# Performance work log

Measured on AMD Instinct MI355X. Metric: run time of the kernel, lower is better.

Reference implementation:

```python
import jax, jax.numpy as jnp
import numpy as np

L = 16384      # sequence length
D_IN = 512     # d_input
D_H = 1024     # d_hidden
D_OUT = 512    # d_output
R_MIN = 0.0
R_MAX = 0.99
MAX_PHASE = np.pi


def setup_inputs() -> dict:
    key = jax.random.key(0)
    k_nu, k_th, k_x, k_bre, k_bim, k_cre, k_cim, k_d = jax.random.split(key, 8)
    # nu_init with parametrization='exp'
    u_nu = jax.random.uniform(k_nu, (D_H,), dtype=jnp.float32)
    nu = jnp.sqrt(u_nu * (R_MAX ** 2 - R_MIN ** 2) + R_MIN ** 2)
    u_theta = jax.random.uniform(k_th, (D_H,), dtype=jnp.float32, minval=-MAX_PHASE, maxval=MAX_PHASE)
    theta = jnp.mod(u_theta, 2 * jnp.pi)
    lamb = jnp.stack([jnp.log(-jnp.log(nu)), jnp.log(theta)], axis=0)  # [2, D_H]
    # gamma_init with parametrization='exp': nu = exp(-exp(lamb[0]))
    nu_eff = jnp.exp(-jnp.exp(lamb[0]))
    gamma = jnp.log(jnp.sqrt(1.0 - jnp.abs(nu_eff) ** 2))  # [D_H]
    # matrix_init: normal / sqrt(shape[0])
    B_re = jax.random.normal(k_bre, (D_H, D_IN), dtype=jnp.float32) / jnp.sqrt(D_H)
    B_im = jax.random.normal(k_bim, (D_H, D_IN), dtype=jnp.float32) / jnp.sqrt(D_H)
    C_re = jax.random.normal(k_cre, (D_OUT, D_H), dtype=jnp.float32) / jnp.sqrt(D_OUT)
    C_im = jax.random.normal(k_cim, (D_OUT, D_H), dtype=jnp.float32) / jnp.sqrt(D_OUT)
    D = jax.random.normal(k_d, (D_OUT, D_IN), dtype=jnp.float32) / jnp.sqrt(D_OUT)
    inputs = jax.random.normal(k_x, (L, D_IN), dtype=jnp.float32)
    return {"inputs": inputs, "lamb": lamb, "gamma": gamma,
            "B_re": B_re, "B_im": B_im, "C_re": C_re, "C_im": C_im, "D": D}


def _binary_operator_diag(q_i, q_j):
    A_i, b_i = q_i
    A_j, b_j = q_j
    return (A_j * A_i, A_j * b_i + b_j)


def reference(inputs, lamb, gamma, B_re, B_im, C_re, C_im, D):
    # parametrization='exp': lambda = exp(-exp(nu_log) + i*exp(theta_log))
    diag_lambda = jnp.exp(-jnp.exp(lamb[0]) + 1j * jnp.exp(lamb[1]))  # [D_H] complex64
    # which_gamma='learned', exp param: scale rows of B by exp(gamma)
    B_norm = jnp.exp(gamma)[:, None] * (B_re + 1j * B_im)             # [D_H, D_IN]
    # Bu_t = B_norm @ x_t for all t, as one GEMM: [L, D_H] complex
    Bu = inputs.astype(B_norm.dtype) @ B_norm.T
    Lambda_elements = jnp.broadcast_to(diag_lambda[None, :], Bu.shape)
    # diagonal linear recurrence h_t = lambda*h_{t-1} + Bu_t via parallel scan
    _, h = jax.lax.associative_scan(_binary_operator_diag, (Lambda_elements, Bu))
    C = C_re + 1j * C_im
    # y_t = Re[C h_t] + D x_t
    outputs = jnp.real(h @ C.T) + inputs @ D.T  # [L, D_OUT]
    return outputs
```

## Files before the change

kernel.cpp:

```cpp
#include <hip/hip_runtime.h>

__device__ __forceinline__ unsigned short f2b(float f) {
    unsigned int u = __builtin_bit_cast(unsigned int, f);
    unsigned int r = (u + 0x7FFFu + ((u >> 16) & 1u)) >> 16;
    return (unsigned short)r;
}
__device__ __forceinline__ float b2f(unsigned short s) {
    unsigned int u = ((unsigned int)s) << 16;
    return __builtin_bit_cast(float, u);
}

typedef __attribute__((ext_vector_type(8))) short short8;
typedef __attribute__((ext_vector_type(4))) float float4v;

#define GLD16(g, l) __builtin_amdgcn_global_load_lds(                          \
    (const __attribute__((address_space(1))) unsigned int*)(g),                \
    (__attribute__((address_space(3))) unsigned int*)(l), 16, 0, 0)

#define WAIT_VMN(n)  __builtin_amdgcn_s_waitcnt(0x0F70 | (n))
#define SB()         __builtin_amdgcn_sched_barrier(0)
#define BAR()        __builtin_amdgcn_s_barrier()

#define SEQLEN 16384
#define NCHUNK 512
#define TCHUNK 32
#define LDH 2560

__global__ void prep_all(const float* __restrict__ x,
                         const float* __restrict__ B_re, const float* __restrict__ B_im,
                         const float* __restrict__ gamma,
                         const float* __restrict__ C_re, const float* __restrict__ C_im,
                         const float* __restrict__ Dm,
                         unsigned short* __restrict__ Hcat,
                         unsigned short* __restrict__ Bcat,
                         unsigned short* __restrict__ CW,
                         float* __restrict__ Yzero) {
    int b = blockIdx.x;
    if (b < 8192) {
        int id = b * 256 + threadIdx.x;
        int t = id >> 7;
        int k4 = (id & 127) << 2;
        float4 v = *(const float4*)(x + (long)t * 512 + k4);
        ushort4 o;
        o.x = f2b(v.x); o.y = f2b(v.y); o.z = f2b(v.z); o.w = f2b(v.w);
        *(ushort4*)(Hcat + (long)t * LDH + 2048 + k4) = o;
    } else if (b < 9216) {
        int id = (b - 8192) * 256 + threadIdx.x;
        int n = id >> 7;
        int k4 = (id & 127) << 2;
        const float* src = (n < 1024) ? (B_re + (long)n * 512) : (B_im + (long)(n - 1024) * 512);
        float g = expf(gamma[n & 1023]);
        float4 v = *(const float4*)(src + k4);
        ushort4 o;
        o.x = f2b(v.x * g); o.y = f2b(v.y * g); o.z = f2b(v.z * g); o.w = f2b(v.w * g);
        *(ushort4*)(Bcat + (long)n * 512 + k4) = o;
    } else if (b < 10496) {
        int id = (b - 9216) * 256 + threadIdx.x;
        int o = id / 640;
        int j4 = (id - o * 640) << 2;
        float4 v; float sgn = 1.0f;
        if (j4 < 1024) {
            v = *(const float4*)(C_re + (long)o * 1024 + j4);
        } else if (j4 < 2048) {
            v = *(const float4*)(C_im + (long)o * 1024 + (j4 - 1024));
            sgn = -1.0f;
        } else {
            v = *(const float4*)(Dm + (long)o * 512 + (j4 - 2048));
        }
        ushort4 w;
        w.x = f2b(v.x * sgn); w.y = f2b(v.y * sgn); w.z = f2b(v.z * sgn); w.w = f2b(v.w * sgn);
        *(ushort4*)(CW + (long)o * 2560 + j4) = w;
    } else {
        int id = (b - 10496) * 256 + threadIdx.x;
        float4 z = {0.0f, 0.0f, 0.0f, 0.0f};
        *(float4*)(Yzero + (long)id * 4) = z;
    }
}

template <int EPI>
__device__ __forceinline__ void gemm256_body(
        const unsigned short* __restrict__ A, int lda,
        const unsigned short* __restrict__ B, int ldb,
        void* __restrict__ Cout, int ldc,
        int nk, long kbase, long m0, long n0) {
    constexpr int ASH = 16384;
    __shared__ unsigned short sm[2][32768] __attribute__((aligned(16)));

    const int tid  = threadIdx.x;
    const int lane = tid & 63;
    const int wid  = tid >> 6;
    const int wr   = wid >> 2;
    const int wc   = wid & 3;

    const int sr = lane >> 3;
    const int sc = ((lane & 7) ^ sr) << 3;
    const unsigned short* Agl = A + (m0 + sr) * (long)lda + sc + kbase;
    const unsigned short* Bgl = B + (n0 + sr) * (long)ldb + sc + kbase;

    const int fr = lane & 15;
    const int x7 = fr & 7;
    const int k0off = (((lane >> 4)    ) ^ x7) << 3;
    const int k1off = (((lane >> 4) + 4) ^ x7) << 3;

    float4v acc[8][4] = {};
    short8 fa[4][2];
    short8 fb[4][2];

    auto stageB = [&](unsigned short* buf, long kt) {
        unsigned short* ldsB = buf + ASH + wid * 512;
        const unsigned short* gB = Bgl + kt;
#pragma unroll
        for (int i = 0; i < 4; i++)
            GLD16(gB + (long)(8 * (wid + 8 * i)) * ldb, ldsB + i * 4096);
    };
    auto stageA = [&](unsigned short* buf, long kt) {
        unsigned short* ldsA = buf + wid * 512;
        const unsigned short* gA = Agl + kt;
#pragma unroll
        for (int i = 0; i < 4; i++)
            GLD16(gA + (long)(8 * (wid + 8 * i)) * lda, ldsA + i * 4096);
    };
    auto ldA = [&](const unsigned short* buf, int mbase) {
#pragma unroll
        for (int i = 0; i < 4; i++) {
            const unsigned short* p = buf + (wr * 128 + (mbase + i) * 16 + fr) * 64;
            fa[i][0] = *(const short8*)(p + k0off);
            fa[i][1] = *(const short8*)(p + k1off);
        }
    };
    auto ldB = [&](const unsigned short* buf, int nbase) {
#pragma unroll
        for (int j = 0; j < 2; j++) {
            const unsigned short* p = buf + ASH + (wc * 64 + (nbase + j) * 16 + fr) * 64;
            fb[nbase + j][0] = *(const short8*)(p + k0off);
            fb[nbase + j][1] = *(const short8*)(p + k1off);
        }
    };
    auto mfmaQ = [&](int mbase, int nbase) {
        __builtin_amdgcn_s_setprio(1);
#pragma unroll
        for (int i = 0; i < 4; i++)
#pragma unroll
            for (int j = 0; j < 2; j++) {
                acc[mbase + i][nbase + j] = __builtin_amdgcn_mfma_f32_16x16x32_bf16(
                    fa[i][0], fb[nbase + j][0], acc[mbase + i][nbase + j], 0, 0, 0);
                acc[mbase + i][nbase + j] = __builtin_amdgcn_mfma_f32_16x16x32_bf16(
                    fa[i][1], fb[nbase + j][1], acc[mbase + i][nbase + j], 0, 0, 0);
            }
        __builtin_amdgcn_s_setprio(0);
    };

    stageB(sm[0], 0);  stageA(sm[0], 0);
    stageB(sm[1], 64); stageA(sm[1], 64);
    WAIT_VMN(8);
    SB(); BAR(); SB();

    for (int t = 0; t < nk; ++t) {
        unsigned short* cur = sm[t & 1];
        const bool st = (t + 2 < nk);
        const long kt2 = (long)(t + 2) * 64;
        ldA(cur, 0); ldB(cur, 0);
        SB(); BAR(); SB();
        mfmaQ(0, 0);
        SB(); BAR(); SB();
        ldB(cur, 2);
        SB(); BAR(); SB();
        mfmaQ(0, 2);
        SB(); BAR(); SB();
        if (st) stageB(cur, kt2);
        ldA(cur, 4);
        SB(); BAR(); SB();
        mfmaQ(4, 0);
        SB(); BAR(); SB();
        if (st) stageA(cur, kt2);
        SB();
        mfmaQ(4, 2);
        if (st)              WAIT_VMN(8);
        else if (t + 1 < nk) WAIT_VMN(0);
        SB(); BAR(); SB();
    }

    const int er = (lane >> 4) * 4;
    const int ec = lane & 15;
#pragma unroll
    for (int mi = 0; mi < 8; mi++) {
#pragma unroll
        for (int r = 0; r < 4; r++) {
            long grow = m0 + wr * 128 + mi * 16 + er + r;
#pragma unroll
            for (int nj = 0; nj < 4; nj++) {
                long gcol = n0 + wc * 64 + nj * 16 + ec;
                float v = acc[mi][nj][r];
                if (EPI == 0)
                    ((unsigned short*)Cout)[grow * ldc + gcol] = f2b(v);
                else
                    atomicAdd(&((float*)Cout)[grow * ldc + gcol], v);
            }
        }
    }
}

__global__ __launch_bounds__(512, 1)
void gemm_bu(const unsigned short* __restrict__ A, int lda,
             const unsigned short* __restrict__ B, int ldb,
             void* __restrict__ Cout, int ldc) {
    const int bid = blockIdx.x;
    const int l = (bid & 7) * 64 + (bid >> 3);
    const long m0 = (long)(l >> 3) * 256;
    const long n0 = (long)(l & 7) * 256;
    gemm256_body<0>(A, lda, B, ldb, Cout, ldc, 8, 0, m0, n0);
}

__global__ __launch_bounds__(512, 1)
void gemm_y(const unsigned short* __restrict__ A, int lda,
            const unsigned short* __restrict__ B, int ldb,
            void* __restrict__ Cout, int ldc) {
    const int bid = blockIdx.x;
    const int l = (bid & 7) * 32 + (bid >> 3);
    const long kbase = (long)(l & 1) * 1280;
    const long n0 = (long)((l >> 1) & 1) * 256;
    const long m0 = (long)(l >> 2) * 256;
    gemm256_body<1>(A, lda, B, ldb, Cout, ldc, 20, kbase, m0, n0);
}

__global__ void scan_ends(const unsigned short* __restrict__ Hcat,
                          const float* __restrict__ lamb,
                          float* __restrict__ E) {
    const int chunk = blockIdx.x;
    const int ch = threadIdx.x << 2;
    float lre[4], lim[4];
#pragma unroll
    for (int i = 0; i < 4; i++) {
        float nu = expf(-expf(lamb[ch + i]));
        float th = expf(lamb[1024 + ch + i]);
        lre[i] = nu * cosf(th);
        lim[i] = nu * sinf(th);
    }
    float hr[4] = {0, 0, 0, 0}, hi[4] = {0, 0, 0, 0};
    const unsigned short* base = Hcat + (long)chunk * TCHUNK * LDH + ch;
#pragma unroll 4
    for (int t = 0; t < TCHUNK; t++) {
        ushort4 br = *(const ushort4*)(base + (long)t * LDH);
        ushort4 bi = *(const ushort4*)(base + (long)t * LDH + 1024);
        float brf[4] = {b2f(br.x), b2f(br.y), b2f(br.z), b2f(br.w)};
        float bif[4] = {b2f(bi.x), b2f(bi.y), b2f(bi.z), b2f(bi.w)};
#pragma unroll
        for (int i = 0; i < 4; i++) {
            float nr = fmaf(lre[i], hr[i], fmaf(-lim[i], hi[i], brf[i]));
            float ni = fmaf(lre[i], hi[i], fmaf(lim[i], hr[i], bif[i]));
            hr[i] = nr; hi[i] = ni;
        }
    }
    float* Ec = E + (long)chunk * 2048 + ch;
#pragma unroll
    for (int i = 0; i < 4; i++) {
        Ec[i] = hr[i];
        Ec[1024 + i] = hi[i];
    }
}

__global__ void carry(const float* __restrict__ lamb, const float* __restrict__ E,
                      float* __restrict__ Kc) {
    const int lane = threadIdx.x & 63;
    const int ch = blockIdx.x * 4 + (threadIdx.x >> 6);
    double nu = exp(-exp((double)lamb[ch]));
    double th = exp((double)lamb[1024 + ch]);
    double lr = nu * cos(th), li = nu * sin(th);
#pragma unroll
    for (int i = 0; i < 5; i++) {
        double rr = lr * lr - li * li;
        double ii = 2.0 * lr * li;
        lr = rr; li = ii;
    }
    const float tre = (float)lr, tim = (float)li;
    double ar = lr, ai = li;
#pragma unroll
    for (int i = 0; i < 3; i++) {
        double rr = ar * ar - ai * ai;
        double ii = 2.0 * ar * ai;
        ar = rr; ai = ii;
    }
    float Ar = (float)ar, Ai = (float)ai;

    const int c0 = lane * 8;
    float er[8], ei[8];
#pragma unroll
    for (int j = 0; j < 8; j++) {
        er[j] = E[(long)(c0 + j) * 2048 + ch];
        ei[j] = E[(long)(c0 + j) * 2048 + 1024 + ch];
    }
    float hr = 0.0f, hi = 0.0f;
#pragma unroll
    for (int j = 0; j < 8; j++) {
        float nr = fmaf(tre, hr, fmaf(-tim, hi, er[j]));
        float ni = fmaf(tre, hi, fmaf(tim, hr, ei[j]));
        hr = nr; hi = ni;
    }
#pragma unroll
    for (int o = 1; o < 64; o <<= 1) {
        float pr = __shfl_up(hr, o);
        float pi = __shfl_up(hi, o);
        float qr = __shfl_up(Ar, o);
        float qi = __shfl_up(Ai, o);
        if (lane >= o) {
            float nr = fmaf(Ar, pr, fmaf(-Ai, pi, hr));
            float ni = fmaf(Ar, pi, fmaf(Ai, pr, hi));
            hr = nr; hi = ni;
            float nar = Ar * qr - Ai * qi;
            float nai = Ar * qi + Ai * qr;
            Ar = nar; Ai = nai;
        }
    }
    float sr = __shfl_up(hr, 1);
    float si = __shfl_up(hi, 1);
    if (lane == 0) { sr = 0.0f; si = 0.0f; }
#pragma unroll
    for (int j = 0; j < 8; j++) {
        Kc[(long)(c0 + j) * 2048 + ch] = sr;
        Kc[(long)(c0 + j) * 2048 + 1024 + ch] = si;
        float nr = fmaf(tre, sr, fmaf(-tim, si, er[j]));
        float ni = fmaf(tre, si, fmaf(tim, sr, ei[j]));
        sr = nr; si = ni;
    }
}

__global__ void scan_apply(unsigned short* __restrict__ Hcat,
                           const float* __restrict__ lamb,
                           const float* __restrict__ Kc) {
    const int chunk = blockIdx.x;
    const int ch = threadIdx.x << 2;
    float lre[4], lim[4];
#pragma unroll
    for (int i = 0; i < 4; i++) {
        float nu = expf(-expf(lamb[ch + i]));
        float th = expf(lamb[1024 + ch + i]);
        lre[i] = nu * cosf(th);
        lim[i] = nu * sinf(th);
    }
    float hr[4], hi[4];
#pragma unroll
    for (int i = 0; i < 4; i++) {
        hr[i] = Kc[(long)chunk * 2048 + ch + i];
        hi[i] = Kc[(long)chunk * 2048 + 1024 + ch + i];
    }
    unsigned short* base = Hcat + (long)chunk * TCHUNK * LDH + ch;
#pragma unroll 4
    for (int t = 0; t < TCHUNK; t++) {
        ushort4 br = *(const ushort4*)(base + (long)t * LDH);
        ushort4 bi = *(const ushort4*)(base + (long)t * LDH + 1024);
        float brf[4] = {b2f(br.x), b2f(br.y), b2f(br.z), b2f(br.w)};
        float bif[4] = {b2f(bi.x), b2f(bi.y), b2f(bi.z), b2f(bi.w)};
#pragma unroll
        for (int i = 0; i < 4; i++) {
            float nr = fmaf(lre[i], hr[i], fmaf(-lim[i], hi[i], brf[i]));
            float ni = fmaf(lre[i], hi[i], fmaf(lim[i], hr[i], bif[i]));
            hr[i] = nr; hi[i] = ni;
        }
        ushort4 orv, oiv;
        orv.x = f2b(hr[0]); orv.y = f2b(hr[1]); orv.z = f2b(hr[2]); orv.w = f2b(hr[3]);
        oiv.x = f2b(hi[0]); oiv.y = f2b(hi[1]); oiv.z = f2b(hi[2]); oiv.w = f2b(hi[3]);
        *(ushort4*)(base + (long)t * LDH) = orv;
        *(ushort4*)(base + (long)t * LDH + 1024) = oiv;
    }
}

extern "C" void kernel_launch(void* const* d_in, const int* in_sizes, int n_in,
                              void* d_out, int out_size, void* d_ws, size_t ws_size,
                              hipStream_t stream) {
    const float* x     = (const float*)d_in[0];
    const float* lamb  = (const float*)d_in[1];
    const float* gamma = (const float*)d_in[2];
    const float* B_re  = (const float*)d_in[3];
    const float* B_im  = (const float*)d_in[4];
    const float* C_re  = (const float*)d_in[5];
    const float* C_im  = (const float*)d_in[6];
    const float* Dm    = (const float*)d_in[7];

    char* ws = (char*)d_ws;
    unsigned short* Hcat = (unsigned short*)ws;
    float* E  = (float*)(ws + 83886080);
    float* Kc = E + (long)NCHUNK * 2048;
    unsigned short* Bcat = (unsigned short*)((char*)Kc + 4194304);
    unsigned short* CW   = Bcat + (long)2048 * 512;

    prep_all<<<12544, 256, 0, stream>>>(x, B_re, B_im, gamma, C_re, C_im, Dm,
                                        Hcat, Bcat, CW, (float*)d_out);
    gemm_bu<<<512, 512, 0, stream>>>(Hcat + 2048, LDH, Bcat, 512, Hcat, LDH);
    scan_ends<<<NCHUNK, 256, 0, stream>>>(Hcat, lamb, E);
    carry<<<256, 256, 0, stream>>>(lamb, E, Kc);
    scan_apply<<<NCHUNK, 256, 0, stream>>>(Hcat, lamb, Kc);
    gemm_y<<<256, 512, 0, stream>>>(Hcat, LDH, CW, 2560, (float*)d_out, 512);
}
```

Before: 274.8 us.

## Fuse scan kernels with grid barrier and drop split-K atomics in output GEMM

```diff
diff --git a/kernel.cpp b/kernel.cpp
--- a/kernel.cpp
+++ b/kernel.cpp
@@ -34,7 +34,7 @@
                          unsigned short* __restrict__ Hcat,
                          unsigned short* __restrict__ Bcat,
                          unsigned short* __restrict__ CW,
-                         float* __restrict__ Yzero) {
+                         unsigned int* __restrict__ ctr) {
     int b = blockIdx.x;
     if (b < 8192) {
         int id = b * 256 + threadIdx.x;
@@ -71,18 +71,14 @@
         w.x = f2b(v.x * sgn); w.y = f2b(v.y * sgn); w.z = f2b(v.z * sgn); w.w = f2b(v.w * sgn);
         *(ushort4*)(CW + (long)o * 2560 + j4) = w;
     } else {
-        int id = (b - 10496) * 256 + threadIdx.x;
-        float4 z = {0.0f, 0.0f, 0.0f, 0.0f};
-        *(float4*)(Yzero + (long)id * 4) = z;
-    }
-}
-
-template <int EPI>
-__device__ __forceinline__ void gemm256_body(
-        const unsigned short* __restrict__ A, int lda,
-        const unsigned short* __restrict__ B, int ldb,
-        void* __restrict__ Cout, int ldc,
-        int nk, long kbase, long m0, long n0) {
+        if (threadIdx.x < 2) ctr[threadIdx.x] = 0u;
+    }
+}
+
+__global__ __launch_bounds__(512, 1)
+void gemm_bu(const unsigned short* __restrict__ A, int lda,
+             const unsigned short* __restrict__ B, int ldb,
+             unsigned short* __restrict__ Cout, int ldc) {
     constexpr int ASH = 16384;
     __shared__ unsigned short sm[2][32768] __attribute__((aligned(16)));
 
@@ -92,10 +88,15 @@
     const int wr   = wid >> 2;
     const int wc   = wid & 3;
 
+    const int bid = blockIdx.x;
+    const int l = (bid & 7) * 64 + (bid >> 3);
+    const long m0 = (long)(l >> 3) * 256;
+    const long n0 = (long)(l & 7) * 256;
+
     const int sr = lane >> 3;
     const int sc = ((lane & 7) ^ sr) << 3;
-    const unsigned short* Agl = A + (m0 + sr) * (long)lda + sc + kbase;
-    const unsigned short* Bgl = B + (n0 + sr) * (long)ldb + sc + kbase;
+    const unsigned short* Agl = A + (m0 + sr) * (long)lda + sc;
+    const unsigned short* Bgl = B + (n0 + sr) * (long)ldb + sc;
 
     const int fr = lane & 15;
     const int x7 = fr & 7;
@@ -150,6 +151,7 @@
         __builtin_amdgcn_s_setprio(0);
     };
 
+    const int nk = 8;
     stageB(sm[0], 0);  stageA(sm[0], 0);
     stageB(sm[1], 64); stageA(sm[1], 64);
     WAIT_VMN(8);
@@ -190,177 +192,283 @@
 #pragma unroll
             for (int nj = 0; nj < 4; nj++) {
                 long gcol = n0 + wc * 64 + nj * 16 + ec;
-                float v = acc[mi][nj][r];
-                if (EPI == 0)
-                    ((unsigned short*)Cout)[grow * ldc + gcol] = f2b(v);
-                else
-                    atomicAdd(&((float*)Cout)[grow * ldc + gcol], v);
-            }
-        }
-    }
-}
-
-__global__ __launch_bounds__(512, 1)
-void gemm_bu(const unsigned short* __restrict__ A, int lda,
-             const unsigned short* __restrict__ B, int ldb,
-             void* __restrict__ Cout, int ldc) {
-    const int bid = blockIdx.x;
-    const int l = (bid & 7) * 64 + (bid >> 3);
-    const long m0 = (long)(l >> 3) * 256;
-    const long n0 = (long)(l & 7) * 256;
-    gemm256_body<0>(A, lda, B, ldb, Cout, ldc, 8, 0, m0, n0);
+                Cout[grow * ldc + gcol] = f2b(acc[mi][nj][r]);
+            }
+        }
+    }
 }
 
 __global__ __launch_bounds__(512, 1)
 void gemm_y(const unsigned short* __restrict__ A, int lda,
             const unsigned short* __restrict__ B, int ldb,
-            void* __restrict__ Cout, int ldc) {
+            float* __restrict__ Cout, int ldc) {
+    constexpr int ASH = 8192;
+    __shared__ unsigned short sm[2][ASH + 16384] __attribute__((aligned(16)));
+
+    const int tid  = threadIdx.x;
+    const int lane = tid & 63;
+    const int wid  = tid >> 6;
+    const int wr   = wid >> 2;
+    const int wc   = wid & 3;
+
     const int bid = blockIdx.x;
-    const int l = (bid & 7) * 32 + (bid >> 3);
-    const long kbase = (long)(l & 1) * 1280;
-    const long n0 = (long)((l >> 1) & 1) * 256;
-    const long m0 = (long)(l >> 2) * 256;
-    gemm256_body<1>(A, lda, B, ldb, Cout, ldc, 20, kbase, m0, n0);
-}
-
-__global__ void scan_ends(const unsigned short* __restrict__ Hcat,
-                          const float* __restrict__ lamb,
-                          float* __restrict__ E) {
+    const int xcd = bid & 7;
+    const int g   = bid >> 3;
+    const int bx  = g & 1;
+    const int by  = xcd * 16 + (g >> 1);
+    const long m0 = (long)by * 128;
+    const long n0 = (long)bx * 256;
+
+    const int sr = lane >> 3;
+    const int sc = ((lane & 7) ^ sr) << 3;
+    const unsigned short* Agl = A + (m0 + sr) * (long)lda + sc;
+    const unsigned short* Bgl = B + (n0 + sr) * (long)ldb + sc;
+
+    const int fr = lane & 15;
+    const int x7 = fr & 7;
+    const int k0off = (((lane >> 4)    ) ^ x7) << 3;
+    const int k1off = (((lane >> 4) + 4) ^ x7) << 3;
+
+    float4v acc[4][4] = {};
+    short8 fa[2][2];
+    short8 fb[4][2];
+
+    auto stageB = [&](unsigned short* buf, long kt) {
+        unsigned short* ldsB = buf + ASH + wid * 512;
+        const unsigned short* gB = Bgl + kt;
+#pragma unroll
+        for (int i = 0; i < 4; i++)
+            GLD16(gB + (long)(8 * (wid + 8 * i)) * ldb, ldsB + i * 4096);
+    };
+    auto stageA = [&](unsigned short* buf, long kt) {
+        unsigned short* ldsA = buf + wid * 512;
+        const unsigned short* gA = Agl + kt;
+#pragma unroll
+        for (int i = 0; i < 2; i++)
+            GLD16(gA + (long)(8 * (wid + 8 * i)) * lda, ldsA + i * 4096);
+    };
+    auto ldA = [&](const unsigned short* buf, int mbase) {
+#pragma unroll
+        for (int i = 0; i < 2; i++) {
+            const unsigned short* p = buf + (wr * 64 + (mbase + i) * 16 + fr) * 64;
+            fa[i][0] = *(const short8*)(p + k0off);
+            fa[i][1] = *(const short8*)(p + k1off);
+        }
+    };
+    auto ldB = [&](const unsigned short* buf, int nbase) {
+#pragma unroll
+        for (int j = 0; j < 2; j++) {
+            const unsigned short* p = buf + ASH + (wc * 64 + (nbase + j) * 16 + fr) * 64;
+            fb[nbase + j][0] = *(const short8*)(p + k0off);
+            fb[nbase + j][1] = *(const short8*)(p + k1off);
+        }
+    };
+    auto mfmaQ = [&](int mbase, int nbase) {
+        __builtin_amdgcn_s_setprio(1);
+#pragma unroll
+        for (int i = 0; i < 2; i++)
+#pragma unroll
+            for (int j = 0; j < 2; j++) {
+                acc[mbase + i][nbase + j] = __builtin_amdgcn_mfma_f32_16x16x32_bf16(
+                    fa[i][0], fb[nbase + j][0], acc[mbase + i][nbase + j], 0, 0, 0);
+                acc[mbase + i][nbase + j] = __builtin_amdgcn_mfma_f32_16x16x32_bf16(
+                    fa[i][1], fb[nbase + j][1], acc[mbase + i][nbase + j], 0, 0, 0);
+            }
+        __builtin_amdgcn_s_setprio(0);
+    };
+
+    const int nk = 40;
+    stageB(sm[0], 0);  stageA(sm[0], 0);
+    stageB(sm[1], 64); stageA(sm[1], 64);
+    WAIT_VMN(6);
+    SB(); BAR(); SB();
+
+    for (int t = 0; t < nk; ++t) {
+        unsigned short* cur = sm[t & 1];
+        const bool st = (t + 2 < nk);
+        const long kt2 = (long)(t + 2) * 64;
+        ldA(cur, 0); ldB(cur, 0);
+        SB(); BAR(); SB();
+        mfmaQ(0, 0);
+        SB(); BAR(); SB();
+        ldB(cur, 2);
+        SB(); BAR(); SB();
+        mfmaQ(0, 2);
+        SB(); BAR(); SB();
+        if (st) stageB(cur, kt2);
+        ldA(cur, 2);
+        SB(); BAR(); SB();
+        mfmaQ(2, 0);
+        SB(); BAR(); SB();
+        if (st) stageA(cur, kt2);
+        SB();
+        mfmaQ(2, 2);
+        if (st)              WAIT_VMN(6);
+        else if (t + 1 < nk) WAIT_VMN(0);
+        SB(); BAR(); SB();
+    }
+
+    const int er = (lane >> 4) * 4;
+    const int ec = lane & 15;
+#pragma unroll
+    for (int mi = 0; mi < 4; mi++) {
+#pragma unroll
+        for (int r = 0; r < 4; r++) {
+            long grow = m0 + wr * 64 + mi * 16 + er + r;
+#pragma unroll
+            for (int nj = 0; nj < 4; nj++) {
+                long gcol = n0 + wc * 64 + nj * 16 + ec;
+                Cout[grow * ldc + gcol] = acc[mi][nj][r];
+            }
+        }
+    }
+}
+
+__device__ __forceinline__ void gbar(unsigned int* c, unsigned int tgt) {
+    __threadfence();
+    __syncthreads();
+    if (threadIdx.x == 0) {
+        atomicAdd(c, 1u);
+        while (__hip_atomic_load(c, __ATOMIC_ACQUIRE, __HIP_MEMORY_SCOPE_AGENT) < tgt)
+            __builtin_amdgcn_s_sleep(2);
+    }
+    __syncthreads();
+    __threadfence();
+}
+
+__global__ __launch_bounds__(256)
+void scan_fused(unsigned short* __restrict__ Hcat,
+                const float* __restrict__ lamb,
+                float* __restrict__ E, float* __restrict__ Kc,
+                unsigned int* __restrict__ ctr) {
     const int chunk = blockIdx.x;
-    const int ch = threadIdx.x << 2;
+    const int ch4 = threadIdx.x << 2;
     float lre[4], lim[4];
 #pragma unroll
     for (int i = 0; i < 4; i++) {
-        float nu = expf(-expf(lamb[ch + i]));
-        float th = expf(lamb[1024 + ch + i]);
+        float nu = expf(-expf(lamb[ch4 + i]));
+        float th = expf(lamb[1024 + ch4 + i]);
         lre[i] = nu * cosf(th);
         lim[i] = nu * sinf(th);
     }
-    float hr[4] = {0, 0, 0, 0}, hi[4] = {0, 0, 0, 0};
-    const unsigned short* base = Hcat + (long)chunk * TCHUNK * LDH + ch;
+
+    unsigned short* base = Hcat + (long)chunk * TCHUNK * LDH + ch4;
+    {
+        float hr[4] = {0, 0, 0, 0}, hi[4] = {0, 0, 0, 0};
 #pragma unroll 4
-    for (int t = 0; t < TCHUNK; t++) {
-        ushort4 br = *(const ushort4*)(base + (long)t * LDH);
-        ushort4 bi = *(const ushort4*)(base + (long)t * LDH + 1024);
-        float brf[4] = {b2f(br.x), b2f(br.y), b2f(br.z), b2f(br.w)};
-        float bif[4] = {b2f(bi.x), b2f(bi.y), b2f(bi.z), b2f(bi.w)};
+        for (int t = 0; t < TCHUNK; t++) {
+            ushort4 br = *(const ushort4*)(base + (long)t * LDH);
+            ushort4 bi = *(const ushort4*)(base + (long)t * LDH + 1024);
+            float brf[4] = {b2f(br.x), b2f(br.y), b2f(br.z), b2f(br.w)};
+            float bif[4] = {b2f(bi.x), b2f(bi.y), b2f(bi.z), b2f(bi.w)};
+#pragma unroll
+            for (int i = 0; i < 4; i++) {
+                float nr = fmaf(lre[i], hr[i], fmaf(-lim[i], hi[i], brf[i]));
+                float ni = fmaf(lre[i], hi[i], fmaf(lim[i], hr[i], bif[i]));
+                hr[i] = nr; hi[i] = ni;
+            }
+        }
+        float* Ec = E + (long)chunk * 2048 + ch4;
 #pragma unroll
         for (int i = 0; i < 4; i++) {
-            float nr = fmaf(lre[i], hr[i], fmaf(-lim[i], hi[i], brf[i]));
-            float ni = fmaf(lre[i], hi[i], fmaf(lim[i], hr[i], bif[i]));
-            hr[i] = nr; hi[i] = ni;
-        }
-    }
-    float* Ec = E + (long)chunk * 2048 + ch;
-#pragma unroll
-    for (int i = 0; i < 4; i++) {
-        Ec[i] = hr[i];
-        Ec[1024 + i] = hi[i];
-    }
-}
-
-__global__ void carry(const float* __restrict__ lamb, const float* __restrict__ E,
-                      float* __restrict__ Kc) {
-    const int lane = threadIdx.x & 63;
-    const int ch = blockIdx.x * 4 + (threadIdx.x >> 6);
-    double nu = exp(-exp((double)lamb[ch]));
-    double th = exp((double)lamb[1024 + ch]);
-    double lr = nu * cos(th), li = nu * sin(th);
-#pragma unroll
-    for (int i = 0; i < 5; i++) {
-        double rr = lr * lr - li * li;
-        double ii = 2.0 * lr * li;
-        lr = rr; li = ii;
-    }
-    const float tre = (float)lr, tim = (float)li;
-    double ar = lr, ai = li;
-#pragma unroll
-    for (int i = 0; i < 3; i++) {
-        double rr = ar * ar - ai * ai;
-        double ii = 2.0 * ar * ai;
-        ar = rr; ai = ii;
-    }
-    float Ar = (float)ar, Ai = (float)ai;
-
-    const int c0 = lane * 8;
-    float er[8], ei[8];
-#pragma unroll
-    for (int j = 0; j < 8; j++) {
-        er[j] = E[(long)(c0 + j) * 2048 + ch];
-        ei[j] = E[(long)(c0 + j) * 2048 + 1024 + ch];
-    }
-    float hr = 0.0f, hi = 0.0f;
-#pragma unroll
-    for (int j = 0; j < 8; j++) {
-        float nr = fmaf(tre, hr, fmaf(-tim, hi, er[j]));
-        float ni = fmaf(tre, hi, fmaf(tim, hr, ei[j]));
-        hr = nr; hi = ni;
-    }
-#pragma unroll
-    for (int o = 1; o < 64; o <<= 1) {
-        float pr = __shfl_up(hr, o);
-        float pi = __shfl_up(hi, o);
-        float qr = __shfl_up(Ar, o);
-        float qi = __shfl_up(Ai, o);
-        if (lane >= o) {
-            float nr = fmaf(Ar, pr, fmaf(-Ai, pi, hr));
-            float ni = fmaf(Ar, pi, fmaf(Ai, pr, hi));
+            Ec[i] = hr[i];
+            Ec[1024 + i] = hi[i];
+        }
+    }
+
+    gbar(ctr + 0, NCHUNK);
+
+    if (chunk < 256) {
+        const int lane = threadIdx.x & 63;
+        const int ch = chunk * 4 + (threadIdx.x >> 6);
+        double nu = exp(-exp((double)lamb[ch]));
+        double th = exp((double)lamb[1024 + ch]);
+        double lr = nu * cos(th), li = nu * sin(th);
+#pragma unroll
+        for (int i = 0; i < 5; i++) {
+            double rr = lr * lr - li * li;
+            double ii = 2.0 * lr * li;
+            lr = rr; li = ii;
+        }
+        const float tre = (float)lr, tim = (float)li;
+        double ar = lr, ai = li;
+#pragma unroll
+        for (int i = 0; i < 3; i++) {
+            double rr = ar * ar - ai * ai;
+            double ii = 2.0 * ar * ai;
+            ar = rr; ai = ii;
+        }
+        float Ar = (float)ar, Ai = (float)ai;
+
+        const int c0 = lane * 8;
+        float er[8], ei[8];
+#pragma unroll
+        for (int j = 0; j < 8; j++) {
+            er[j] = E[(long)(c0 + j) * 2048 + ch];
+            ei[j] = E[(long)(c0 + j) * 2048 + 1024 + ch];
+        }
+        float hr = 0.0f, hi = 0.0f;
+#pragma unroll
+        for (int j = 0; j < 8; j++) {
+            float nr = fmaf(tre, hr, fmaf(-tim, hi, er[j]));
+            float ni = fmaf(tre, hi, fmaf(tim, hr, ei[j]));
             hr = nr; hi = ni;
-            float nar = Ar * qr - Ai * qi;
-            float nai = Ar * qi + Ai * qr;
-            Ar = nar; Ai = nai;
-        }
-    }
-    float sr = __shfl_up(hr, 1);
-    float si = __shfl_up(hi, 1);
-    if (lane == 0) { sr = 0.0f; si = 0.0f; }
-#pragma unroll
-    for (int j = 0; j < 8; j++) {
-        Kc[(long)(c0 + j) * 2048 + ch] = sr;
-        Kc[(long)(c0 + j) * 2048 + 1024 + ch] = si;
-        float nr = fmaf(tre, sr, fmaf(-tim, si, er[j]));
-        float ni = fmaf(tre, si, fmaf(tim, sr, ei[j]));
-        sr = nr; si = ni;
-    }
-}
-
-__global__ void scan_apply(unsigned short* __restrict__ Hcat,
-                           const float* __restrict__ lamb,
-                           const float* __restrict__ Kc) {
-    const int chunk = blockIdx.x;
-    const int ch = threadIdx.x << 2;
-    float lre[4], lim[4];
-#pragma unroll
-    for (int i = 0; i < 4; i++) {
-        float nu = expf(-expf(lamb[ch + i]));
-        float th = expf(lamb[1024 + ch + i]);
-        lre[i] = nu * cosf(th);
-        lim[i] = nu * sinf(th);
-    }
-    float hr[4], hi[4];
-#pragma unroll
-    for (int i = 0; i < 4; i++) {
-        hr[i] = Kc[(long)chunk * 2048 + ch + i];
-        hi[i] = Kc[(long)chunk * 2048 + 1024 + ch + i];
-    }
-    unsigned short* base = Hcat + (long)chunk * TCHUNK * LDH + ch;
+        }
+#pragma unroll
+        for (int o = 1; o < 64; o <<= 1) {
+            float pr = __shfl_up(hr, o);
+            float pi = __shfl_up(hi, o);
+            float qr = __shfl_up(Ar, o);
+            float qi = __shfl_up(Ai, o);
+            if (lane >= o) {
+                float nr = fmaf(Ar, pr, fmaf(-Ai, pi, hr));
+                float ni = fmaf(Ar, pi, fmaf(Ai, pr, hi));
+                hr = nr; hi = ni;
+                float nar = Ar * qr - Ai * qi;
+                float nai = Ar * qi + Ai * qr;
+                Ar = nar; Ai = nai;
+            }
+        }
+        float sr = __shfl_up(hr, 1);
+        float si = __shfl_up(hi, 1);
+        if (lane == 0) { sr = 0.0f; si = 0.0f; }
+#pragma unroll
+        for (int j = 0; j < 8; j++) {
+            Kc[(long)(c0 + j) * 2048 + ch] = sr;
+            Kc[(long)(c0 + j) * 2048 + 1024 + ch] = si;
+            float nr = fmaf(tre, sr, fmaf(-tim, si, er[j]));
+            float ni = fmaf(tre, si, fmaf(tim, sr, ei[j]));
+            sr = nr; si = ni;
+        }
+    }
+
+    gbar(ctr + 1, NCHUNK);
+
+    {
+        float hr[4], hi[4];
+#pragma unroll
+        for (int i = 0; i < 4; i++) {
+            hr[i] = Kc[(long)chunk * 2048 + ch4 + i];
+            hi[i] = Kc[(long)chunk * 2048 + 1024 + ch4 + i];
+        }
 #pragma unroll 4
-    for (int t = 0; t < TCHUNK; t++) {
-        ushort4 br = *(const ushort4*)(base + (long)t * LDH);
-        ushort4 bi = *(const ushort4*)(base + (long)t * LDH + 1024);
-        float brf[4] = {b2f(br.x), b2f(br.y), b2f(br.z), b2f(br.w)};
-        float bif[4] = {b2f(bi.x), b2f(bi.y), b2f(bi.z), b2f(bi.w)};
-#pragma unroll
-        for (int i = 0; i < 4; i++) {
-            float nr = fmaf(lre[i], hr[i], fmaf(-lim[i], hi[i], brf[i]));
-            float ni = fmaf(lre[i], hi[i], fmaf(lim[i], hr[i], bif[i]));
-            hr[i] = nr; hi[i] = ni;
-        }
-        ushort4 orv, oiv;
-        orv.x = f2b(hr[0]); orv.y = f2b(hr[1]); orv.z = f2b(hr[2]); orv.w = f2b(hr[3]);
-        oiv.x = f2b(hi[0]); oiv.y = f2b(hi[1]); oiv.z = f2b(hi[2]); oiv.w = f2b(hi[3]);
-        *(ushort4*)(base + (long)t * LDH) = orv;
-        *(ushort4*)(base + (long)t * LDH + 1024) = oiv;
+        for (int t = 0; t < TCHUNK; t++) {
+            ushort4 br = *(const ushort4*)(base + (long)t * LDH);
+            ushort4 bi = *(const ushort4*)(base + (long)t * LDH + 1024);
+            float brf[4] = {b2f(br.x), b2f(br.y), b2f(br.z), b2f(br.w)};
+            float bif[4] = {b2f(bi.x), b2f(bi.y), b2f(bi.z), b2f(bi.w)};
+#pragma unroll
+            for (int i = 0; i < 4; i++) {
+                float nr = fmaf(lre[i], hr[i], fmaf(-lim[i], hi[i], brf[i]));
+                float ni = fmaf(lre[i], hi[i], fmaf(lim[i], hr[i], bif[i]));
+                hr[i] = nr; hi[i] = ni;
+            }
+            ushort4 orv, oiv;
+            orv.x = f2b(hr[0]); orv.y = f2b(hr[1]); orv.z = f2b(hr[2]); orv.w = f2b(hr[3]);
+            oiv.x = f2b(hi[0]); oiv.y = f2b(hi[1]); oiv.z = f2b(hi[2]); oiv.w = f2b(hi[3]);
+            *(ushort4*)(base + (long)t * LDH) = orv;
+            *(ushort4*)(base + (long)t * LDH + 1024) = oiv;
+        }
     }
 }
 
@@ -382,12 +490,11 @@
     float* Kc = E + (long)NCHUNK * 2048;
     unsigned short* Bcat = (unsigned short*)((char*)Kc + 4194304);
     unsigned short* CW   = Bcat + (long)2048 * 512;
-
-    prep_all<<<12544, 256, 0, stream>>>(x, B_re, B_im, gamma, C_re, C_im, Dm,
-                                        Hcat, Bcat, CW, (float*)d_out);
+    unsigned int* ctr    = (unsigned int*)((char*)CW + 2621440);
+
+    prep_all<<<10497, 256, 0, stream>>>(x, B_re, B_im, gamma, C_re, C_im, Dm,
+                                        Hcat, Bcat, CW, ctr);
     gemm_bu<<<512, 512, 0, stream>>>(Hcat + 2048, LDH, Bcat, 512, Hcat, LDH);
-    scan_ends<<<NCHUNK, 256, 0, stream>>>(Hcat, lamb, E);
-    carry<<<256, 256, 0, stream>>>(lamb, E, Kc);
-    scan_apply<<<NCHUNK, 256, 0, stream>>>(Hcat, lamb, Kc);
+    scan_fused<<<NCHUNK, 256, 0, stream>>>(Hcat, lamb, E, Kc, ctr);
     gemm_y<<<256, 512, 0, stream>>>(Hcat, LDH, CW, 2560, (float*)d_out, 512);
 }
```

Result: slower. 514.3 us (+87.2%).
